# Performance work log

Hardware: AMD Instinct MI355X
Metric: run time of the kernel (lower is better)

## Reference

```python
import jax, jax.numpy as jnp
import numpy as np

B, T, D, H = 2, 2048, 1024, 16
HD = D // H

def setup_inputs() -> dict:
    key = jax.random.key(0)
    ks = jax.random.split(key, 5)
    fan = D
    bound_w = float(np.sqrt(6.0 / fan))  # kaiming_uniform-ish scale
    return {
        "x": jax.random.normal(ks[0], (B, T, D), dtype=jnp.float32),
        "W_qkv": jax.random.uniform(ks[1], (3 * D, D), minval=-bound_w, maxval=bound_w, dtype=jnp.float32),
        "b_qkv": jax.random.uniform(ks[2], (3 * D,), minval=-bound_w, maxval=bound_w, dtype=jnp.float32),
        "W_proj": jax.random.uniform(ks[3], (D, D), minval=-bound_w, maxval=bound_w, dtype=jnp.float32),
        "b_proj": jax.random.uniform(ks[4], (D,), minval=-bound_w, maxval=bound_w, dtype=jnp.float32),
    }

def reference(x, W_qkv, b_qkv, W_proj, b_proj):
    Bx, Tx, C = x.shape
    h, hd = H, C // H
    qkv = x @ W_qkv.T + b_qkv                      # (B,T,3C)
    q, k, v = jnp.split(qkv, 3, axis=-1)
    # (B,T,C) -> (B,h,T,hd)
    q = q.reshape(Bx, Tx, h, hd).transpose(0, 2, 1, 3)
    k = k.reshape(Bx, Tx, h, hd).transpose(0, 2, 1, 3)
    v = v.reshape(Bx, Tx, h, hd).transpose(0, 2, 1, 3)
    scale = hd ** -0.5
    scores = jnp.einsum('bhqd,bhkd->bhqk', q, k) * scale
    causal = jnp.tril(jnp.ones((Tx, Tx), dtype=bool))
    scores = jnp.where(causal, scores, -jnp.inf)
    weights = jax.nn.softmax(scores, axis=-1)      # stable softmax, same math
    out = jnp.einsum('bhqk,bhkd->bhqd', weights, v)
    out = out.transpose(0, 2, 1, 3).reshape(Bx, Tx, C)
    return out @ W_proj.T + b_proj
```

## Files before the change

### kernel.cpp

```cpp
#include <hip/hip_runtime.h>

typedef unsigned short u16;
typedef __attribute__((ext_vector_type(8))) short bf16x8;
typedef __attribute__((ext_vector_type(4))) float f32x4;

#define Bb 2
#define Tt 2048
#define Dd 1024
#define Hh 16
#define HD 64
#define NTOK (Bb*Tt)

__device__ __forceinline__ u16 f2b(float f) {
    unsigned u = __float_as_uint(f);
    unsigned r = (u + 0x7fffu + ((u >> 16) & 1u)) >> 16;
    return (u16)r;
}

__device__ __forceinline__ void g2l16(const u16* g, u16* l) {
    __builtin_amdgcn_global_load_lds(
        (const __attribute__((address_space(1))) unsigned int*)g,
        (__attribute__((address_space(3))) unsigned int*)l,
        16, 0, 0);
}

__device__ __forceinline__ unsigned pk2(float lo, float hi) {
    return __builtin_amdgcn_perm(__float_as_uint(hi), __float_as_uint(lo), 0x07060302u);
}

#define N4X  (NTOK * Dd / 4)
#define N4WQ (3 * Dd * Dd / 4)
#define N4WP (Dd * Dd / 4)
__global__ void cvt_all(const float* __restrict__ x, const float* __restrict__ wq,
                        const float* __restrict__ wp, u16* __restrict__ xb,
                        u16* __restrict__ wqb, u16* __restrict__ wpb) {
    int i = blockIdx.x * blockDim.x + threadIdx.x;
    const float* src; u16* dst; int j;
    if (i < N4X)                { src = x;  dst = xb;  j = i; }
    else if (i < N4X + N4WQ)    { src = wq; dst = wqb; j = i - N4X; }
    else                        { src = wp; dst = wpb; j = i - N4X - N4WQ; }
    float4 f = ((const float4*)src)[j];
    ushort4 o;
    o.x = f2b(f.x); o.y = f2b(f.y); o.z = f2b(f.z); o.w = f2b(f.w);
    ((ushort4*)dst)[j] = o;
}

template<int MODE>
__global__ __launch_bounds__(256, 2)
void gemm_bt(const u16* __restrict__ A, const u16* __restrict__ Bt,
             const float* __restrict__ bias, int M, int N, int K,
             u16* __restrict__ Qo, u16* __restrict__ Ko, u16* __restrict__ Vo,
             float* __restrict__ Co) {
    __shared__ alignas(16) u16 As[128 * 32];
    __shared__ alignas(16) u16 Bs[128 * 32];
    const int tid = threadIdx.x;
    const int wave = tid >> 6, lane = tid & 63;
    const int quad = lane >> 4, l16 = lane & 15;
    const int wm = (wave & 1) * 64, wn = (wave >> 1) * 64;
    const int m0 = blockIdx.x * 128, n0 = blockIdx.y * 128;
    const int lrow = lane >> 2, lcol = (lane & 3) << 3;

    f32x4 acc[4][4];
#pragma unroll
    for (int i = 0; i < 4; ++i)
#pragma unroll
        for (int j = 0; j < 4; ++j)
            acc[i][j] = (f32x4){0.f, 0.f, 0.f, 0.f};

    for (int k0 = 0; k0 < K; k0 += 32) {
#pragma unroll
        for (int c = 0; c < 2; ++c) {
            const int rb = (c * 4 + wave) * 16;
            g2l16(A  + (size_t)(m0 + rb + lrow) * K + k0 + lcol, &As[rb * 32 + (lane << 3)]);
            g2l16(Bt + (size_t)(n0 + rb + lrow) * K + k0 + lcol, &Bs[rb * 32 + (lane << 3)]);
        }
        __syncthreads();
        bf16x8 a[4], b[4];
#pragma unroll
        for (int i = 0; i < 4; ++i)
            a[i] = *(const bf16x8*)(&As[(wm + i * 16 + l16) * 32 + quad * 8]);
#pragma unroll
        for (int i = 0; i < 4; ++i)
            b[i] = *(const bf16x8*)(&Bs[(wn + i * 16 + l16) * 32 + quad * 8]);
#pragma unroll
        for (int i = 0; i < 4; ++i)
#pragma unroll
            for (int j = 0; j < 4; ++j)
                acc[i][j] = __builtin_amdgcn_mfma_f32_16x16x32_bf16(a[i], b[j], acc[i][j], 0, 0, 0);
        __syncthreads();
    }

#pragma unroll
    for (int i = 0; i < 4; ++i) {
#pragma unroll
        for (int j = 0; j < 4; ++j) {
#pragma unroll
            for (int r = 0; r < 4; ++r) {
                int m = m0 + wm + i * 16 + quad * 4 + r;
                int n = n0 + wn + j * 16 + l16;
                float v = acc[i][j][r] + bias[n];
                if (MODE == 0) {
                    u16 bv = f2b(v);
                    int bidx = m >> 11, t = m & 2047;
                    int s = n >> 10, c = n & 1023;
                    int hh = c >> 6, d = c & 63;
                    size_t base = (size_t)(bidx * Hh + hh);
                    u16* dst = (s == 0) ? Qo : (s == 1) ? Ko : Vo;
                    dst[(base * Tt + t) * HD + d] = bv;
                } else {
                    Co[(size_t)m * N + n] = v;
                }
            }
        }
    }
}

__global__ __launch_bounds__(256)
void transpose_v(const u16* __restrict__ V, u16* __restrict__ Vt) {
    __shared__ u16 Ls[64 * 66];
    const int t0 = blockIdx.x * 64, bh = blockIdx.y;
    const int tid = threadIdx.x;
    const int r = tid >> 2, c = (tid & 3) << 4;
    const u16* src = V + ((size_t)bh * Tt + t0 + r) * HD + c;
    *(uint4*)(&Ls[r * 66 + c]) = *(const uint4*)src;
    *(uint4*)(&Ls[r * 66 + c + 8]) = *(const uint4*)(src + 8);
    __syncthreads();
    const int d = tid >> 2, tc = (tid & 3) << 4;
    u16 tmp[16];
#pragma unroll
    for (int j = 0; j < 16; ++j) tmp[j] = Ls[(tc + j) * 66 + d];
    u16* dst = Vt + ((size_t)bh * HD + d) * Tt + t0 + tc;
    *(uint4*)(dst)     = *(const uint4*)(tmp);
    *(uint4*)(dst + 8) = *(const uint4*)(tmp + 8);
}

#define LKP 80
#define PSP 80
#define FMX 24.0f

__global__ __launch_bounds__(256, 4)
void attn_fwd(const u16* __restrict__ Q, const u16* __restrict__ Kg,
              const u16* __restrict__ Vt, u16* __restrict__ Ao) {
    const int pair = blockIdx.x, bh = blockIdx.y;
    const u16* Qp = Q + (size_t)bh * Tt * HD;
    const u16* Kp = Kg + (size_t)bh * Tt * HD;
    const u16* Vp = Vt + (size_t)bh * HD * Tt;
    const int tid = threadIdx.x;
    const int wave = tid >> 6, lane = tid & 63;
    const int quad = lane >> 4, l16 = lane & 15;
    const int hh = bh & (Hh - 1), bidx = bh >> 4;

    __shared__ alignas(16) u16 Ks[64 * LKP];
    __shared__ alignas(16) u16 Vs[64 * LKP];
    __shared__ alignas(16) u16 Ps[4][16 * PSP];
    u16* Pw = &Ps[wave][0];

    const int srow = tid >> 3, scol = (tid & 7) << 3;
    const float sc = 0.125f * 1.44269504f;

    for (int half = 0; half < 2; ++half) {
        const int qt = half ? pair : (31 - pair);
        const int q0 = qt * 64;
        const int qrow_g = q0 + wave * 16 + l16;
        bf16x8 aq[2];
#pragma unroll
        for (int kk = 0; kk < 2; ++kk)
            aq[kk] = *(const bf16x8*)(Qp + (size_t)qrow_g * HD + kk * 32 + quad * 8);

        f32x4 o[4];
#pragma unroll
        for (int nt = 0; nt < 4; ++nt) o[nt] = (f32x4){0.f, 0.f, 0.f, 0.f};
        float lsum = 0.f;
        const int nit = qt + 1;

        uint4 kreg0, kreg1, vreg0, vreg1;
        kreg0 = *(const uint4*)(Kp + (size_t)srow * HD + scol);
        kreg1 = *(const uint4*)(Kp + (size_t)(srow + 32) * HD + scol);
        vreg0 = *(const uint4*)(Vp + (size_t)srow * Tt + scol);
        vreg1 = *(const uint4*)(Vp + (size_t)(srow + 32) * Tt + scol);

        for (int kt = 0; kt < nit; ++kt) {
            const int k0 = kt * 64;
            *(uint4*)(&Ks[srow * LKP + scol]) = kreg0;
            *(uint4*)(&Ks[(srow + 32) * LKP + scol]) = kreg1;
            *(uint4*)(&Vs[srow * LKP + scol]) = vreg0;
            *(uint4*)(&Vs[(srow + 32) * LKP + scol]) = vreg1;
            __syncthreads();
            if (kt + 1 < nit) {
                const int kn = k0 + 64;
                kreg0 = *(const uint4*)(Kp + (size_t)(kn + srow) * HD + scol);
                kreg1 = *(const uint4*)(Kp + (size_t)(kn + srow + 32) * HD + scol);
                vreg0 = *(const uint4*)(Vp + (size_t)srow * Tt + kn + scol);
                vreg1 = *(const uint4*)(Vp + (size_t)(srow + 32) * Tt + kn + scol);
            }

            f32x4 s[4];
#pragma unroll
            for (int nt = 0; nt < 4; ++nt) {
                f32x4 z = (f32x4){0.f, 0.f, 0.f, 0.f};
#pragma unroll
                for (int kk = 0; kk < 2; ++kk) {
                    bf16x8 ak = *(const bf16x8*)(&Ks[(nt * 16 + l16) * LKP + kk * 32 + quad * 8]);
                    z = __builtin_amdgcn_mfma_f32_16x16x32_bf16(ak, aq[kk], z, 0, 0, 0);
                }
                s[nt] = z;
            }

            if (kt == qt) {
#pragma unroll
                for (int nt = 0; nt < 4; ++nt)
#pragma unroll
                    for (int r = 0; r < 4; ++r) {
                        int key = k0 + nt * 16 + quad * 4 + r;
                        float t = __builtin_fmaf(s[nt][r], sc, -FMX);
                        t = (key <= qrow_g) ? t : -200.0f;
                        float p = exp2f(t);
                        s[nt][r] = p;
                        lsum += p;
                    }
            } else {
#pragma unroll
                for (int nt = 0; nt < 4; ++nt)
#pragma unroll
                    for (int r = 0; r < 4; ++r) {
                        float p = exp2f(__builtin_fmaf(s[nt][r], sc, -FMX));
                        s[nt][r] = p;
                        lsum += p;
                    }
            }

#pragma unroll
            for (int nt = 0; nt < 4; ++nt) {
                uint2 d;
                d.x = pk2(s[nt][0], s[nt][1]);
                d.y = pk2(s[nt][2], s[nt][3]);
                *(uint2*)(&Pw[l16 * PSP + nt * 16 + quad * 4]) = d;
            }

#pragma unroll
            for (int kk = 0; kk < 2; ++kk) {
                bf16x8 bp = *(const bf16x8*)(&Pw[l16 * PSP + kk * 32 + quad * 8]);
#pragma unroll
                for (int nt = 0; nt < 4; ++nt) {
                    bf16x8 av = *(const bf16x8*)(&Vs[(nt * 16 + l16) * LKP + kk * 32 + quad * 8]);
                    o[nt] = __builtin_amdgcn_mfma_f32_16x16x32_bf16(av, bp, o[nt], 0, 0, 0);
                }
            }
            __syncthreads();
        }

        lsum += __shfl_xor(lsum, 16, 64);
        lsum += __shfl_xor(lsum, 32, 64);
        const float rinv = 1.0f / lsum;
        u16* orow = Ao + ((size_t)bidx * Tt + qrow_g) * Dd + hh * HD;
#pragma unroll
        for (int nt = 0; nt < 4; ++nt) {
            ushort4 p4;
            p4.x = f2b(o[nt][0] * rinv); p4.y = f2b(o[nt][1] * rinv);
            p4.z = f2b(o[nt][2] * rinv); p4.w = f2b(o[nt][3] * rinv);
            *(ushort4*)(orow + nt * 16 + quad * 4) = p4;
        }
    }
}

extern "C" void kernel_launch(void* const* d_in, const int* in_sizes, int n_in,
                              void* d_out, int out_size, void* d_ws, size_t ws_size,
                              hipStream_t stream) {
    const float* x      = (const float*)d_in[0];
    const float* W_qkv  = (const float*)d_in[1];
    const float* b_qkv  = (const float*)d_in[2];
    const float* W_proj = (const float*)d_in[3];
    const float* b_proj = (const float*)d_in[4];
    float* out = (float*)d_out;

    char* ws = (char*)d_ws;
    u16* xb     = (u16*)(ws);
    u16* Wqkvb  = (u16*)(ws + (8u << 20));
    u16* Wprojb = (u16*)(ws + (14u << 20));
    u16* Qb     = (u16*)(ws + (16u << 20));
    u16* Kb     = (u16*)(ws + (24u << 20));
    u16* Vb     = (u16*)(ws + (32u << 20));
    u16* attnb  = (u16*)(ws + (40u << 20));
    u16* Vtb    = xb;

    cvt_all<<<(N4X + N4WQ + N4WP) / 256, 256, 0, stream>>>(x, W_qkv, W_proj, xb, Wqkvb, Wprojb);

    {
        dim3 grid(NTOK / 128, (3 * Dd) / 128);
        gemm_bt<0><<<grid, 256, 0, stream>>>(xb, Wqkvb, b_qkv, NTOK, 3 * Dd, Dd,
                                             Qb, Kb, Vb, nullptr);
    }
    {
        dim3 grid(Tt / 64, Bb * Hh);
        transpose_v<<<grid, 256, 0, stream>>>(Vb, Vtb);
    }
    {
        dim3 grid(Tt / 128, Bb * Hh);
        attn_fwd<<<grid, 256, 0, stream>>>(Qb, Kb, Vtb, attnb);
    }
    {
        dim3 grid(NTOK / 128, Dd / 128);
        gemm_bt<1><<<grid, 256, 0, stream>>>(attnb, Wprojb, b_proj, NTOK, Dd, Dd,
                                             nullptr, nullptr, nullptr, out);
    }
}
```

Before: 193.7 us.

## Store QKV row-major, read Q/K strided in attention, one q-tile per block

The QKV GEMM now writes a plain row-major (token, 3*D) bf16 buffer instead of scattering into per-head Q/K/V layouts. The V transpose and attention kernels index into this packed buffer with a row stride of 3*D. Attention blocks now handle a single query tile each (grid of 32 per head, heaviest tiles first) instead of pairing a long and a short tile. Other changes: bias values are hoisted into registers in the GEMM epilogue, the P-tile LDS pitch is padded, and workspace buffers are reassigned. The row-major epilogue is meant to cut the scatter cost, but strided Q/K reads and the unbalanced single-tile blocks may cost attention efficiency.

```diff
diff --git a/kernel.cpp b/kernel.cpp
--- a/kernel.cpp
+++ b/kernel.cpp
@@ -10,6 +10,7 @@
 #define Hh 16
 #define HD 64
 #define NTOK (Bb*Tt)
+#define QKVN (3*Dd)
 
 __device__ __forceinline__ u16 f2b(float f) {
     unsigned u = __float_as_uint(f);
@@ -49,8 +50,7 @@
 __global__ __launch_bounds__(256, 2)
 void gemm_bt(const u16* __restrict__ A, const u16* __restrict__ Bt,
              const float* __restrict__ bias, int M, int N, int K,
-             u16* __restrict__ Qo, u16* __restrict__ Ko, u16* __restrict__ Vo,
-             float* __restrict__ Co) {
+             u16* __restrict__ C16, float* __restrict__ Co) {
     __shared__ alignas(16) u16 As[128 * 32];
     __shared__ alignas(16) u16 Bs[128 * 32];
     const int tid = threadIdx.x;
@@ -90,6 +90,10 @@
         __syncthreads();
     }
 
+    float b4[4];
+#pragma unroll
+    for (int j = 0; j < 4; ++j) b4[j] = bias[n0 + wn + j * 16 + l16];
+
 #pragma unroll
     for (int i = 0; i < 4; ++i) {
 #pragma unroll
@@ -98,30 +102,22 @@
             for (int r = 0; r < 4; ++r) {
                 int m = m0 + wm + i * 16 + quad * 4 + r;
                 int n = n0 + wn + j * 16 + l16;
-                float v = acc[i][j][r] + bias[n];
-                if (MODE == 0) {
-                    u16 bv = f2b(v);
-                    int bidx = m >> 11, t = m & 2047;
-                    int s = n >> 10, c = n & 1023;
-                    int hh = c >> 6, d = c & 63;
-                    size_t base = (size_t)(bidx * Hh + hh);
-                    u16* dst = (s == 0) ? Qo : (s == 1) ? Ko : Vo;
-                    dst[(base * Tt + t) * HD + d] = bv;
-                } else {
-                    Co[(size_t)m * N + n] = v;
-                }
+                float v = acc[i][j][r] + b4[j];
+                if (MODE == 0) C16[(size_t)m * N + n] = f2b(v);
+                else           Co[(size_t)m * N + n] = v;
             }
         }
     }
 }
 
 __global__ __launch_bounds__(256)
-void transpose_v(const u16* __restrict__ V, u16* __restrict__ Vt) {
+void transpose_v(const u16* __restrict__ qkv, u16* __restrict__ Vt) {
     __shared__ u16 Ls[64 * 66];
     const int t0 = blockIdx.x * 64, bh = blockIdx.y;
+    const int hh = bh & (Hh - 1), bidx = bh >> 4;
     const int tid = threadIdx.x;
     const int r = tid >> 2, c = (tid & 3) << 4;
-    const u16* src = V + ((size_t)bh * Tt + t0 + r) * HD + c;
+    const u16* src = qkv + (size_t)(bidx * Tt + t0 + r) * QKVN + 2 * Dd + hh * HD + c;
     *(uint4*)(&Ls[r * 66 + c]) = *(const uint4*)src;
     *(uint4*)(&Ls[r * 66 + c + 8]) = *(const uint4*)(src + 8);
     __syncthreads();
@@ -135,20 +131,21 @@
 }
 
 #define LKP 80
-#define PSP 80
+#define PSP 84
 #define FMX 24.0f
 
 __global__ __launch_bounds__(256, 4)
-void attn_fwd(const u16* __restrict__ Q, const u16* __restrict__ Kg,
-              const u16* __restrict__ Vt, u16* __restrict__ Ao) {
-    const int pair = blockIdx.x, bh = blockIdx.y;
-    const u16* Qp = Q + (size_t)bh * Tt * HD;
-    const u16* Kp = Kg + (size_t)bh * Tt * HD;
+void attn_fwd(const u16* __restrict__ qkv, const u16* __restrict__ Vt,
+              u16* __restrict__ Ao) {
+    const int qt = 31 - (int)blockIdx.x;
+    const int bh = blockIdx.y;
+    const int hh = bh & (Hh - 1), bidx = bh >> 4;
+    const u16* Qp = qkv + (size_t)bidx * Tt * QKVN + hh * HD;
+    const u16* Kp = Qp + Dd;
     const u16* Vp = Vt + (size_t)bh * HD * Tt;
     const int tid = threadIdx.x;
     const int wave = tid >> 6, lane = tid & 63;
     const int quad = lane >> 4, l16 = lane & 15;
-    const int hh = bh & (Hh - 1), bidx = bh >> 4;
 
     __shared__ alignas(16) u16 Ks[64 * LKP];
     __shared__ alignas(16) u16 Vs[64 * LKP];
@@ -158,108 +155,105 @@
     const int srow = tid >> 3, scol = (tid & 7) << 3;
     const float sc = 0.125f * 1.44269504f;
 
-    for (int half = 0; half < 2; ++half) {
-        const int qt = half ? pair : (31 - pair);
-        const int q0 = qt * 64;
-        const int qrow_g = q0 + wave * 16 + l16;
-        bf16x8 aq[2];
-#pragma unroll
-        for (int kk = 0; kk < 2; ++kk)
-            aq[kk] = *(const bf16x8*)(Qp + (size_t)qrow_g * HD + kk * 32 + quad * 8);
-
-        f32x4 o[4];
-#pragma unroll
-        for (int nt = 0; nt < 4; ++nt) o[nt] = (f32x4){0.f, 0.f, 0.f, 0.f};
-        float lsum = 0.f;
-        const int nit = qt + 1;
-
-        uint4 kreg0, kreg1, vreg0, vreg1;
-        kreg0 = *(const uint4*)(Kp + (size_t)srow * HD + scol);
-        kreg1 = *(const uint4*)(Kp + (size_t)(srow + 32) * HD + scol);
-        vreg0 = *(const uint4*)(Vp + (size_t)srow * Tt + scol);
-        vreg1 = *(const uint4*)(Vp + (size_t)(srow + 32) * Tt + scol);
-
-        for (int kt = 0; kt < nit; ++kt) {
-            const int k0 = kt * 64;
-            *(uint4*)(&Ks[srow * LKP + scol]) = kreg0;
-            *(uint4*)(&Ks[(srow + 32) * LKP + scol]) = kreg1;
-            *(uint4*)(&Vs[srow * LKP + scol]) = vreg0;
-            *(uint4*)(&Vs[(srow + 32) * LKP + scol]) = vreg1;
-            __syncthreads();
-            if (kt + 1 < nit) {
-                const int kn = k0 + 64;
-                kreg0 = *(const uint4*)(Kp + (size_t)(kn + srow) * HD + scol);
-                kreg1 = *(const uint4*)(Kp + (size_t)(kn + srow + 32) * HD + scol);
-                vreg0 = *(const uint4*)(Vp + (size_t)srow * Tt + kn + scol);
-                vreg1 = *(const uint4*)(Vp + (size_t)(srow + 32) * Tt + kn + scol);
+    const int q0 = qt * 64;
+    const int qrow_g = q0 + wave * 16 + l16;
+    bf16x8 aq[2];
+#pragma unroll
+    for (int kk = 0; kk < 2; ++kk)
+        aq[kk] = *(const bf16x8*)(Qp + (size_t)qrow_g * QKVN + kk * 32 + quad * 8);
+
+    f32x4 o[4];
+#pragma unroll
+    for (int nt = 0; nt < 4; ++nt) o[nt] = (f32x4){0.f, 0.f, 0.f, 0.f};
+    float lsum = 0.f;
+    const int nit = qt + 1;
+
+    uint4 kreg0, kreg1, vreg0, vreg1;
+    kreg0 = *(const uint4*)(Kp + (size_t)srow * QKVN + scol);
+    kreg1 = *(const uint4*)(Kp + (size_t)(srow + 32) * QKVN + scol);
+    vreg0 = *(const uint4*)(Vp + (size_t)srow * Tt + scol);
+    vreg1 = *(const uint4*)(Vp + (size_t)(srow + 32) * Tt + scol);
+
+    for (int kt = 0; kt < nit; ++kt) {
+        const int k0 = kt * 64;
+        *(uint4*)(&Ks[srow * LKP + scol]) = kreg0;
+        *(uint4*)(&Ks[(srow + 32) * LKP + scol]) = kreg1;
+        *(uint4*)(&Vs[srow * LKP + scol]) = vreg0;
+        *(uint4*)(&Vs[(srow + 32) * LKP + scol]) = vreg1;
+        __syncthreads();
+        if (kt + 1 < nit) {
+            const int kn = k0 + 64;
+            kreg0 = *(const uint4*)(Kp + (size_t)(kn + srow) * QKVN + scol);
+            kreg1 = *(const uint4*)(Kp + (size_t)(kn + srow + 32) * QKVN + scol);
+            vreg0 = *(const uint4*)(Vp + (size_t)srow * Tt + kn + scol);
+            vreg1 = *(const uint4*)(Vp + (size_t)(srow + 32) * Tt + kn + scol);
+        }
+
+        f32x4 s[4];
+#pragma unroll
+        for (int nt = 0; nt < 4; ++nt) {
+            f32x4 z = (f32x4){0.f, 0.f, 0.f, 0.f};
+#pragma unroll
+            for (int kk = 0; kk < 2; ++kk) {
+                bf16x8 ak = *(const bf16x8*)(&Ks[(nt * 16 + l16) * LKP + kk * 32 + quad * 8]);
+                z = __builtin_amdgcn_mfma_f32_16x16x32_bf16(ak, aq[kk], z, 0, 0, 0);
             }
-
-            f32x4 s[4];
+            s[nt] = z;
+        }
+
+        if (kt == qt) {
+#pragma unroll
+            for (int nt = 0; nt < 4; ++nt)
+#pragma unroll
+                for (int r = 0; r < 4; ++r) {
+                    int key = k0 + nt * 16 + quad * 4 + r;
+                    float t = __builtin_fmaf(s[nt][r], sc, -FMX);
+                    t = (key <= qrow_g) ? t : -200.0f;
+                    float p = exp2f(t);
+                    s[nt][r] = p;
+                    lsum += p;
+                }
+        } else {
+#pragma unroll
+            for (int nt = 0; nt < 4; ++nt)
+#pragma unroll
+                for (int r = 0; r < 4; ++r) {
+                    float p = exp2f(__builtin_fmaf(s[nt][r], sc, -FMX));
+                    s[nt][r] = p;
+                    lsum += p;
+                }
+        }
+
+#pragma unroll
+        for (int nt = 0; nt < 4; ++nt) {
+            uint2 d;
+            d.x = pk2(s[nt][0], s[nt][1]);
+            d.y = pk2(s[nt][2], s[nt][3]);
+            *(uint2*)(&Pw[l16 * PSP + nt * 16 + quad * 4]) = d;
+        }
+
+#pragma unroll
+        for (int kk = 0; kk < 2; ++kk) {
+            bf16x8 bp = *(const bf16x8*)(&Pw[l16 * PSP + kk * 32 + quad * 8]);
 #pragma unroll
             for (int nt = 0; nt < 4; ++nt) {
-                f32x4 z = (f32x4){0.f, 0.f, 0.f, 0.f};
-#pragma unroll
-                for (int kk = 0; kk < 2; ++kk) {
-                    bf16x8 ak = *(const bf16x8*)(&Ks[(nt * 16 + l16) * LKP + kk * 32 + quad * 8]);
-                    z = __builtin_amdgcn_mfma_f32_16x16x32_bf16(ak, aq[kk], z, 0, 0, 0);
-                }
-                s[nt] = z;
+                bf16x8 av = *(const bf16x8*)(&Vs[(nt * 16 + l16) * LKP + kk * 32 + quad * 8]);
+                o[nt] = __builtin_amdgcn_mfma_f32_16x16x32_bf16(av, bp, o[nt], 0, 0, 0);
             }
-
-            if (kt == qt) {
-#pragma unroll
-                for (int nt = 0; nt < 4; ++nt)
-#pragma unroll
-                    for (int r = 0; r < 4; ++r) {
-                        int key = k0 + nt * 16 + quad * 4 + r;
-                        float t = __builtin_fmaf(s[nt][r], sc, -FMX);
-                        t = (key <= qrow_g) ? t : -200.0f;
-                        float p = exp2f(t);
-                        s[nt][r] = p;
-                        lsum += p;
-                    }
-            } else {
-#pragma unroll
-                for (int nt = 0; nt < 4; ++nt)
-#pragma unroll
-                    for (int r = 0; r < 4; ++r) {
-                        float p = exp2f(__builtin_fmaf(s[nt][r], sc, -FMX));
-                        s[nt][r] = p;
-                        lsum += p;
-                    }
-            }
-
-#pragma unroll
-            for (int nt = 0; nt < 4; ++nt) {
-                uint2 d;
-                d.x = pk2(s[nt][0], s[nt][1]);
-                d.y = pk2(s[nt][2], s[nt][3]);
-                *(uint2*)(&Pw[l16 * PSP + nt * 16 + quad * 4]) = d;
-            }
-
-#pragma unroll
-            for (int kk = 0; kk < 2; ++kk) {
-                bf16x8 bp = *(const bf16x8*)(&Pw[l16 * PSP + kk * 32 + quad * 8]);
-#pragma unroll
-                for (int nt = 0; nt < 4; ++nt) {
-                    bf16x8 av = *(const bf16x8*)(&Vs[(nt * 16 + l16) * LKP + kk * 32 + quad * 8]);
-                    o[nt] = __builtin_amdgcn_mfma_f32_16x16x32_bf16(av, bp, o[nt], 0, 0, 0);
-                }
-            }
-            __syncthreads();
-        }
-
-        lsum += __shfl_xor(lsum, 16, 64);
-        lsum += __shfl_xor(lsum, 32, 64);
-        const float rinv = 1.0f / lsum;
-        u16* orow = Ao + ((size_t)bidx * Tt + qrow_g) * Dd + hh * HD;
-#pragma unroll
-        for (int nt = 0; nt < 4; ++nt) {
-            ushort4 p4;
-            p4.x = f2b(o[nt][0] * rinv); p4.y = f2b(o[nt][1] * rinv);
-            p4.z = f2b(o[nt][2] * rinv); p4.w = f2b(o[nt][3] * rinv);
-            *(ushort4*)(orow + nt * 16 + quad * 4) = p4;
-        }
+        }
+        __syncthreads();
+    }
+
+    lsum += __shfl_xor(lsum, 16, 64);
+    lsum += __shfl_xor(lsum, 32, 64);
+    const float rinv = 1.0f / lsum;
+    u16* orow = Ao + ((size_t)bidx * Tt + qrow_g) * Dd + hh * HD;
+#pragma unroll
+    for (int nt = 0; nt < 4; ++nt) {
+        ushort4 p4;
+        p4.x = f2b(o[nt][0] * rinv); p4.y = f2b(o[nt][1] * rinv);
+        p4.z = f2b(o[nt][2] * rinv); p4.w = f2b(o[nt][3] * rinv);
+        *(ushort4*)(orow + nt * 16 + quad * 4) = p4;
     }
 }
 
@@ -274,33 +268,31 @@
     float* out = (float*)d_out;
 
     char* ws = (char*)d_ws;
-    u16* xb     = (u16*)(ws);
-    u16* Wqkvb  = (u16*)(ws + (8u << 20));
-    u16* Wprojb = (u16*)(ws + (14u << 20));
-    u16* Qb     = (u16*)(ws + (16u << 20));
-    u16* Kb     = (u16*)(ws + (24u << 20));
-    u16* Vb     = (u16*)(ws + (32u << 20));
-    u16* attnb  = (u16*)(ws + (40u << 20));
-    u16* Vtb    = xb;
+    u16* Wprojb = (u16*)(ws);
+    u16* Wqkvb  = (u16*)(ws + (2u << 20));
+    u16* xb     = (u16*)(ws + (8u << 20));
+    u16* qkvb   = (u16*)(ws + (16u << 20));
+    u16* Vtb    = (u16*)(ws + (40u << 20));
+    u16* attnb  = (u16*)(ws + (2u << 20));
 
     cvt_all<<<(N4X + N4WQ + N4WP) / 256, 256, 0, stream>>>(x, W_qkv, W_proj, xb, Wqkvb, Wprojb);
 
     {
-        dim3 grid(NTOK / 128, (3 * Dd) / 128);
-        gemm_bt<0><<<grid, 256, 0, stream>>>(xb, Wqkvb, b_qkv, NTOK, 3 * Dd, Dd,
-                                             Qb, Kb, Vb, nullptr);
+        dim3 grid(NTOK / 128, QKVN / 128);
+        gemm_bt<0><<<grid, 256, 0, stream>>>(xb, Wqkvb, b_qkv, NTOK, QKVN, Dd,
+                                             qkvb, nullptr);
     }
     {
         dim3 grid(Tt / 64, Bb * Hh);
-        transpose_v<<<grid, 256, 0, stream>>>(Vb, Vtb);
-    }
-    {
-        dim3 grid(Tt / 128, Bb * Hh);
-        attn_fwd<<<grid, 256, 0, stream>>>(Qb, Kb, Vtb, attnb);
+        transpose_v<<<grid, 256, 0, stream>>>(qkvb, Vtb);
+    }
+    {
+        dim3 grid(32, Bb * Hh);
+        attn_fwd<<<grid, 256, 0, stream>>>(qkvb, Vtb, attnb);
     }
     {
         dim3 grid(NTOK / 128, Dd / 128);
         gemm_bt<1><<<grid, 256, 0, stream>>>(attnb, Wprojb, b_proj, NTOK, Dd, Dd,
-                                             nullptr, nullptr, nullptr, out);
-    }
-}
+                                             nullptr, out);
+    }
+}
```

Result: slower. 216.1 us (+11.5%).
